# Kernel tuning notes

Measured on AMD Instinct MI355X. Metric: run time of the kernel, lower is better.

## Reference

```python
import jax, jax.numpy as jnp
import numpy as np

N_NODES = 100000
N_EDGES = 1600000
IN_DIM, HID, OUT_DIM = 128, 64, 1


def _sage_conv(x, src, dst, wl, wr, b, num_nodes):
    # PyG SAGEConv (aggr='mean', root_weight=True):
    #   out = lin_l(mean_{j in N(i)} x_j) + lin_r(x_i), bias lives in lin_l
    msgs = x[src]                                                  # [E, d] gather
    agg = jax.ops.segment_sum(msgs, dst, num_segments=num_nodes)  # [N, d]
    deg = jax.ops.segment_sum(jnp.ones((src.shape[0],), x.dtype), dst,
                              num_segments=num_nodes)              # [N]
    agg = agg / jnp.maximum(deg, 1.0)[:, None]                     # mean aggregation
    return agg @ wl + x @ wr + b


def setup_inputs() -> dict:
    key = jax.random.key(0)
    ks = jax.random.split(key, 12)
    x = jax.random.normal(ks[0], (N_NODES, IN_DIM), dtype=jnp.float32)
    edge_index = jax.random.randint(ks[1], (2, N_EDGES), 0, N_NODES, dtype=jnp.int64)

    def glorot(k, fan_in, fan_out):
        s = jnp.sqrt(2.0 / (fan_in + fan_out)).astype(jnp.float32)
        return jax.random.normal(k, (fan_in, fan_out), dtype=jnp.float32) * s

    return {
        "x": x,
        "edge_index": edge_index,
        "wl0": glorot(ks[2], IN_DIM, HID), "wr0": glorot(ks[3], IN_DIM, HID),
        "b0": jnp.zeros((HID,), jnp.float32),
        "wl1": glorot(ks[4], HID, HID), "wr1": glorot(ks[5], HID, HID),
        "b1": jnp.zeros((HID,), jnp.float32),
        "wl2": glorot(ks[6], HID, OUT_DIM), "wr2": glorot(ks[7], HID, OUT_DIM),
        "b2": jnp.zeros((OUT_DIM,), jnp.float32),
    }


def reference(x, edge_index, wl0, wr0, b0, wl1, wr1, b1, wl2, wr2, b2):
    src, dst = edge_index[0], edge_index[1]
    n = x.shape[0]
    # layer 0: conv -> relu (dropout is identity in eval mode)
    h = jax.nn.relu(_sage_conv(x, src, dst, wl0, wr0, b0, n))
    # layer 1
    h = jax.nn.relu(_sage_conv(h, src, dst, wl1, wr1, b1, n))
    # final layer + sigmoid
    h = _sage_conv(h, src, dst, wl2, wr2, b2, n)
    return jax.nn.sigmoid(h)
```

## Files before the change

### kernel.cpp

```cpp
#include <hip/hip_runtime.h>
#include <hip/hip_bf16.h>
#include <math.h>


#define SHIFT 7
#define BKT 128
#define CHUNK 4096
#define CAP 4096

typedef __bf16 bf16_t;
typedef bf16_t bf16x8 __attribute__((ext_vector_type(8)));
typedef float f32x4 __attribute__((ext_vector_type(4)));

#define B16LO(u) __uint_as_float((u) << 16)
#define B16HI(u) __uint_as_float((u) & 0xffff0000u)

__global__ __launch_bounds__(256) void scatter_prep(const int* __restrict__ srcv,
                                                    const int* __restrict__ dstv,
                                                    int* __restrict__ bcnt,
                                                    int* __restrict__ bucketed,
                                                    int E, int NB, int nbC,
                                                    const float* __restrict__ wl0,
                                                    const float* __restrict__ wr0,
                                                    const float* __restrict__ wl1,
                                                    const float* __restrict__ wr1,
                                                    bf16_t* __restrict__ w0t,
                                                    bf16_t* __restrict__ w1t) {
    if ((int)blockIdx.x >= nbC) {
        int idx = (blockIdx.x - nbC) * 256 + threadIdx.x;
        if (idx < 128 * 128) {
            int j = idx >> 7, k = idx & 127;
            float v = (j < 64) ? wl0[k * 64 + j] : wr0[k * 64 + (j - 64)];
            w0t[idx] = (bf16_t)v;
        } else if (idx < 128 * 128 + 128 * 64) {
            int i2 = idx - 128 * 128;
            int j = i2 >> 6, k = i2 & 63;
            float v = (j < 64) ? wl1[k * 64 + j] : wr1[k * 64 + (j - 64)];
            w1t[i2] = (bf16_t)v;
        }
        return;
    }
    __shared__ int hist[1024];
    __shared__ int offl[1024];
    __shared__ int basel[1024];
    __shared__ int partial[256];
    __shared__ int posA[CHUNK];
    __shared__ int valA[CHUNK];
    const int t = threadIdx.x;
    for (int i = t; i < NB; i += 256) hist[i] = 0;
    __syncthreads();

    const int cbase = blockIdx.x * CHUNK;
    int bk[CHUNK / 256], rk[CHUNK / 256], vv[CHUNK / 256];
#pragma unroll
    for (int k = 0; k < CHUNK / 256; ++k) {
        int e = cbase + t + k * 256;
        if (e < E) {
            int d = dstv[e];
            int s = srcv[e];
            int b = d >> SHIFT;
            bk[k] = b;
            rk[k] = atomicAdd(&hist[b], 1);
            vv[k] = (s << SHIFT) | (d & (BKT - 1));
        } else {
            bk[k] = -1;
        }
    }
    __syncthreads();

    for (int b = t; b < NB; b += 256) {
        int c = hist[b];
        basel[b] = c ? (b * CAP + atomicAdd(&bcnt[b], c)) : 0;
    }
    {
        int g = t * 4;
        int a0 = (g + 0 < NB) ? hist[g + 0] : 0;
        int a1 = (g + 1 < NB) ? hist[g + 1] : 0;
        int a2 = (g + 2 < NB) ? hist[g + 2] : 0;
        int a3 = (g + 3 < NB) ? hist[g + 3] : 0;
        int sum = a0 + a1 + a2 + a3;
        partial[t] = sum;
        __syncthreads();
        for (int d = 1; d < 256; d <<= 1) {
            int x = (t >= d) ? partial[t - d] : 0;
            __syncthreads();
            partial[t] += x;
            __syncthreads();
        }
        int ex = partial[t] - sum;
        if (g + 0 < NB) offl[g + 0] = ex;
        if (g + 1 < NB) offl[g + 1] = ex + a0;
        if (g + 2 < NB) offl[g + 2] = ex + a0 + a1;
        if (g + 3 < NB) offl[g + 3] = ex + a0 + a1 + a2;
    }
    __syncthreads();

    int nloc = E - cbase;
    if (nloc > CHUNK) nloc = CHUNK;
#pragma unroll
    for (int k = 0; k < CHUNK / 256; ++k) {
        if (bk[k] >= 0) {
            int slot = offl[bk[k]] + rk[k];
            posA[slot] = basel[bk[k]] + rk[k];
            valA[slot] = vv[k];
        }
    }
    __syncthreads();
    for (int j = t; j < nloc; j += 256) bucketed[posA[j]] = valA[j];
}

__global__ __launch_bounds__(256) void sort_gemm0(const int* __restrict__ bucketed,
                                                  const int* __restrict__ bcnt,
                                                  int2* __restrict__ od,
                                                  int* __restrict__ csr, int N, int NB,
                                                  const float* __restrict__ x,
                                                  const bf16_t* __restrict__ w0t,
                                                  bf16_t* __restrict__ y) {
    __shared__ int cnt[BKT];
    __shared__ int sc[BKT];
    __shared__ int cur[BKT];
    const int t = threadIdx.x;

    if ((int)blockIdx.x >= NB) {
        const int bid = blockIdx.x - NB;
        const int lane = t & 63;
        const int wv = t >> 6;
        const int r0 = bid * 64 + wv * 16;
        const int rr = lane & 15;
        const int quad = lane >> 4;
        const int row_store = r0 + rr;
        int row = (row_store < N) ? row_store : (N - 1);

        bf16x8 xf[4];
#pragma unroll
        for (int kk = 0; kk < 4; ++kk) {
            const float* ap = &x[(size_t)row * 128 + kk * 32 + quad * 8];
            float4 f0 = *(const float4*)ap;
            float4 f1 = *(const float4*)(ap + 4);
            union { bf16x8 v; bf16_t h[8]; } u;
            u.h[0] = (bf16_t)f0.x; u.h[1] = (bf16_t)f0.y;
            u.h[2] = (bf16_t)f0.z; u.h[3] = (bf16_t)f0.w;
            u.h[4] = (bf16_t)f1.x; u.h[5] = (bf16_t)f1.y;
            u.h[6] = (bf16_t)f1.z; u.h[7] = (bf16_t)f1.w;
            xf[kk] = u.v;
        }
#pragma unroll
        for (int c = 0; c < 8; ++c) {
            f32x4 acc = {0.f, 0.f, 0.f, 0.f};
#pragma unroll
            for (int kk = 0; kk < 4; ++kk) {
                bf16x8 wf = *(const bf16x8*)&w0t[(size_t)(c * 16 + rr) * 128 + kk * 32 + quad * 8];
                acc = __builtin_amdgcn_mfma_f32_16x16x32_bf16(wf, xf[kk], acc, 0, 0, 0);
            }
            if (row_store < N) {
                union { bf16_t h[4]; uint2 u; } p;
                p.h[0] = (bf16_t)acc[0]; p.h[1] = (bf16_t)acc[1];
                p.h[2] = (bf16_t)acc[2]; p.h[3] = (bf16_t)acc[3];
                *(uint2*)&y[(size_t)row_store * 128 + c * 16 + quad * 4] = p.u;
            }
        }
        return;
    }

    const int b = blockIdx.x;
    const int ebase = b * CAP;
    const int eend = ebase + bcnt[b];
    if (t < BKT) cnt[t] = 0;
    __syncthreads();
    int wreg[CAP / 256];
#pragma unroll
    for (int k = 0; k < CAP / 256; ++k) {
        int i = ebase + t + k * 256;
        if (i < eend) {
            wreg[k] = bucketed[i];
            atomicAdd(&cnt[wreg[k] & (BKT - 1)], 1);
        }
    }
    __syncthreads();
    int v = (t < BKT) ? cnt[t] : 0;
    if (t < BKT) sc[t] = v;
    __syncthreads();
    for (int d = 1; d < BKT; d <<= 1) {
        int xsc = (t < BKT && t >= d) ? sc[t - d] : 0;
        __syncthreads();
        if (t < BKT) sc[t] += xsc;
        __syncthreads();
    }
    if (t < BKT) {
        int ex = sc[t] - v;
        cur[t] = ex;
        int dst = (b << SHIFT) + t;
        if (dst < N) od[dst] = make_int2(ebase + ex, v);
    }
    __syncthreads();
#pragma unroll
    for (int k = 0; k < CAP / 256; ++k) {
        int i = ebase + t + k * 256;
        if (i < eend) {
            int w = wreg[k];
            int p = atomicAdd(&cur[w & (BKT - 1)], 1);
            csr[ebase + p] = w >> SHIFT;
        }
    }
}

__global__ __launch_bounds__(256) void gemm1(const bf16_t* __restrict__ A,
                                             const bf16_t* __restrict__ Wt,
                                             bf16_t* __restrict__ Y, int N) {
    const int lane = threadIdx.x & 63;
    const int wv = threadIdx.x >> 6;
    const int r0 = blockIdx.x * 64 + wv * 16;
    const int rr = lane & 15;
    const int quad = lane >> 4;
    const int row_store = r0 + rr;
    int row = (row_store < N) ? row_store : (N - 1);

    bf16x8 xf[2];
#pragma unroll
    for (int kk = 0; kk < 2; ++kk)
        xf[kk] = *(const bf16x8*)&A[(size_t)row * 64 + kk * 32 + quad * 8];

#pragma unroll
    for (int c = 0; c < 8; ++c) {
        f32x4 acc = {0.f, 0.f, 0.f, 0.f};
#pragma unroll
        for (int kk = 0; kk < 2; ++kk) {
            bf16x8 wf = *(const bf16x8*)&Wt[(size_t)(c * 16 + rr) * 64 + kk * 32 + quad * 8];
            acc = __builtin_amdgcn_mfma_f32_16x16x32_bf16(wf, xf[kk], acc, 0, 0, 0);
        }
        if (row_store < N) {
            union { bf16_t h[4]; uint2 u; } p;
            p.h[0] = (bf16_t)acc[0]; p.h[1] = (bf16_t)acc[1];
            p.h[2] = (bf16_t)acc[2]; p.h[3] = (bf16_t)acc[3];
            *(uint2*)&Y[(size_t)row_store * 128 + c * 16 + quad * 4] = p.u;
        }
    }
}

template <bool FUSED>
__global__ __launch_bounds__(256) void agg_relu(const bf16_t* __restrict__ y,
                                                const int* __restrict__ csr,
                                                const int2* __restrict__ od,
                                                const float* __restrict__ bias,
                                                bf16_t* __restrict__ h,
                                                const float* __restrict__ wl2,
                                                const float* __restrict__ wr2,
                                                float* __restrict__ sl,
                                                float* __restrict__ sr, int N) {
    const int lane = threadIdx.x & 63;
    const int oct = lane >> 3;
    const int ch = (lane & 7) * 8;
    const int nw = gridDim.x * 4;

    int i = blockIdx.x * 4 + (threadIdx.x >> 6);
    int2 odc = (i < N) ? od[i] : make_int2(0, 0);
    int sidx = 0;
    if (i < N) sidx = (lane < odc.y) ? csr[odc.x + lane] : 0;

    while (i < N) {
        const int inext = i + nw;
        int2 odn = (inext < N) ? od[inext] : make_int2(0, 0);

        const int base = odc.x;
        const int d = odc.y;
        float a0 = 0.f, a1 = 0.f, a2 = 0.f, a3 = 0.f;
        float a4 = 0.f, a5 = 0.f, a6 = 0.f, a7 = 0.f;
        const int nblk = d >> 3;
        const int pm = (nblk < 8) ? nblk : 8;
        int p = 0;
        for (; p + 2 <= pm; p += 2) {
            int s0 = __shfl(sidx, 8 * p + oct);
            int s1 = __shfl(sidx, 8 * p + 8 + oct);
            uint4 v0 = *(const uint4*)&y[(size_t)s0 * 128 + ch];
            uint4 v1 = *(const uint4*)&y[(size_t)s1 * 128 + ch];
            a0 += B16LO(v0.x) + B16LO(v1.x); a1 += B16HI(v0.x) + B16HI(v1.x);
            a2 += B16LO(v0.y) + B16LO(v1.y); a3 += B16HI(v0.y) + B16HI(v1.y);
            a4 += B16LO(v0.z) + B16LO(v1.z); a5 += B16HI(v0.z) + B16HI(v1.z);
            a6 += B16LO(v0.w) + B16LO(v1.w); a7 += B16HI(v0.w) + B16HI(v1.w);
        }
        for (; p < pm; ++p) {
            int s0 = __shfl(sidx, 8 * p + oct);
            uint4 v0 = *(const uint4*)&y[(size_t)s0 * 128 + ch];
            a0 += B16LO(v0.x); a1 += B16HI(v0.x);
            a2 += B16LO(v0.y); a3 += B16HI(v0.y);
            a4 += B16LO(v0.z); a5 += B16HI(v0.z);
            a6 += B16LO(v0.w); a7 += B16HI(v0.w);
        }
        for (; p < nblk; ++p) {
            int s0 = csr[base + 8 * p + oct];
            uint4 v0 = *(const uint4*)&y[(size_t)s0 * 128 + ch];
            a0 += B16LO(v0.x); a1 += B16HI(v0.x);
            a2 += B16LO(v0.y); a3 += B16HI(v0.y);
            a4 += B16LO(v0.z); a5 += B16HI(v0.z);
            a6 += B16LO(v0.w); a7 += B16HI(v0.w);
        }
        {
            int te = 8 * nblk + oct;
            int tec = (te < 64) ? te : 63;
            int s_t = __shfl(sidx, tec);
            if (te < d) {
                int s0 = (te < 64) ? s_t : csr[base + te];
                uint4 v0 = *(const uint4*)&y[(size_t)s0 * 128 + ch];
                a0 += B16LO(v0.x); a1 += B16HI(v0.x);
                a2 += B16LO(v0.y); a3 += B16HI(v0.y);
                a4 += B16LO(v0.z); a5 += B16HI(v0.z);
                a6 += B16LO(v0.w); a7 += B16HI(v0.w);
            }
        }

        int sidxn = 0;
        if (inext < N) sidxn = (lane < odn.y) ? csr[odn.x + lane] : 0;

        a0 += __shfl_xor(a0, 8);  a1 += __shfl_xor(a1, 8);
        a2 += __shfl_xor(a2, 8);  a3 += __shfl_xor(a3, 8);
        a4 += __shfl_xor(a4, 8);  a5 += __shfl_xor(a5, 8);
        a6 += __shfl_xor(a6, 8);  a7 += __shfl_xor(a7, 8);
        a0 += __shfl_xor(a0, 16); a1 += __shfl_xor(a1, 16);
        a2 += __shfl_xor(a2, 16); a3 += __shfl_xor(a3, 16);
        a4 += __shfl_xor(a4, 16); a5 += __shfl_xor(a5, 16);
        a6 += __shfl_xor(a6, 16); a7 += __shfl_xor(a7, 16);
        a0 += __shfl_xor(a0, 32); a1 += __shfl_xor(a1, 32);
        a2 += __shfl_xor(a2, 32); a3 += __shfl_xor(a3, 32);
        a4 += __shfl_xor(a4, 32); a5 += __shfl_xor(a5, 32);
        a6 += __shfl_xor(a6, 32); a7 += __shfl_xor(a7, 32);

        float inv = 1.f / ((d > 0) ? (float)d : 1.f);
        uint4 vs = *(const uint4*)&y[(size_t)i * 128 + 64 + ch];
        float4 bv0 = *(const float4*)&bias[ch];
        float4 bv1 = *(const float4*)&bias[ch + 4];
        float v0 = fmaxf(a0 * inv + B16LO(vs.x) + bv0.x, 0.f);
        float v1 = fmaxf(a1 * inv + B16HI(vs.x) + bv0.y, 0.f);
        float v2 = fmaxf(a2 * inv + B16LO(vs.y) + bv0.z, 0.f);
        float v3 = fmaxf(a3 * inv + B16HI(vs.y) + bv0.w, 0.f);
        float v4 = fmaxf(a4 * inv + B16LO(vs.z) + bv1.x, 0.f);
        float v5 = fmaxf(a5 * inv + B16HI(vs.z) + bv1.y, 0.f);
        float v6 = fmaxf(a6 * inv + B16LO(vs.w) + bv1.z, 0.f);
        float v7 = fmaxf(a7 * inv + B16HI(vs.w) + bv1.w, 0.f);

        if (!FUSED) {
            if (oct == 0) {
                union { bf16_t b[8]; uint4 u; } pk;
                pk.b[0] = (bf16_t)v0; pk.b[1] = (bf16_t)v1;
                pk.b[2] = (bf16_t)v2; pk.b[3] = (bf16_t)v3;
                pk.b[4] = (bf16_t)v4; pk.b[5] = (bf16_t)v5;
                pk.b[6] = (bf16_t)v6; pk.b[7] = (bf16_t)v7;
                *(uint4*)&h[(size_t)i * 64 + ch] = pk.u;
            }
        } else {
            float4 w0 = *(const float4*)&wl2[ch];
            float4 w1 = *(const float4*)&wl2[ch + 4];
            float4 u0 = *(const float4*)&wr2[ch];
            float4 u1 = *(const float4*)&wr2[ch + 4];
            float a = v0 * w0.x + v1 * w0.y + v2 * w0.z + v3 * w0.w +
                      v4 * w1.x + v5 * w1.y + v6 * w1.z + v7 * w1.w;
            float b = v0 * u0.x + v1 * u0.y + v2 * u0.z + v3 * u0.w +
                      v4 * u1.x + v5 * u1.y + v6 * u1.z + v7 * u1.w;
            a += __shfl_xor(a, 1); b += __shfl_xor(b, 1);
            a += __shfl_xor(a, 2); b += __shfl_xor(b, 2);
            a += __shfl_xor(a, 4); b += __shfl_xor(b, 4);
            if (lane == 0) { sl[i] = a; sr[i] = b; }
        }

        odc = odn;
        sidx = sidxn;
        i = inext;
    }
}

__global__ __launch_bounds__(256) void final_k(const float* __restrict__ sl,
                                               const float* __restrict__ sr,
                                               const int* __restrict__ csr,
                                               const int2* __restrict__ od,
                                               const float* __restrict__ b2,
                                               float* __restrict__ out, int N) {
    int wid = blockIdx.x * 4 + (threadIdx.x >> 6);
    if (wid >= N) return;
    const int lane = threadIdx.x & 63;
    const int2 odv = od[wid];
    const int base = odv.x;
    const int d = odv.y;
    float acc = 0.f;
    for (int e = lane; e < d; e += 64) acc += sl[csr[base + e]];
#pragma unroll
    for (int off = 32; off; off >>= 1) acc += __shfl_xor(acc, off);
    if (lane == 0) {
        float m = (d > 0) ? (float)d : 1.f;
        float v = acc / m + sr[wid] + b2[0];
        out[wid] = 1.f / (1.f + expf(-v));
    }
}

extern "C" void kernel_launch(void* const* d_in, const int* in_sizes, int n_in,
                              void* d_out, int out_size, void* d_ws, size_t ws_size,
                              hipStream_t stream) {
    const float* x  = (const float*)d_in[0];
    const int*  ei  = (const int*)d_in[1];
    const float* wl0 = (const float*)d_in[2];
    const float* wr0 = (const float*)d_in[3];
    const float* b0  = (const float*)d_in[4];
    const float* wl1 = (const float*)d_in[5];
    const float* wr1 = (const float*)d_in[6];
    const float* b1  = (const float*)d_in[7];
    const float* wl2 = (const float*)d_in[8];
    const float* wr2 = (const float*)d_in[9];
    const float* b2  = (const float*)d_in[10];
    float* out = (float*)d_out;

    const int E = in_sizes[1] / 2;
    const int N = out_size;
    const int* srcv = ei;
    const int* dstv = ei + E;
    const int NB = (N + BKT - 1) >> SHIFT;

    char* ws = (char*)d_ws;
    size_t o = 0;
    auto take = [&](size_t nbytes) -> void* {
        void* p = ws + o;
        o = (o + nbytes + 255) & ~(size_t)255;
        return p;
    };
    int2* od      = (int2*)take((size_t)N * 8);
    int* bcnt     = (int*)take((size_t)(NB + 2) * 4);
    int* bucketed = (int*)take((size_t)NB * CAP * 4);
    int* csr      = (int*)take((size_t)NB * CAP * 4);
    bf16_t* w0t   = (bf16_t*)take(128 * 128 * 2);
    bf16_t* w1t   = (bf16_t*)take(128 * 64 * 2);
    bf16_t* y     = (bf16_t*)take((size_t)N * 128 * 2);
    bf16_t* h     = (bf16_t*)take((size_t)N * 64 * 2);
    float* sl     = (float*)take((size_t)N * 4);
    float* sr     = (float*)take((size_t)N * 4);
    (void)ws_size;

    const int nbC = (E + CHUNK - 1) / CHUNK;
    const int nbP = (128 * 128 + 128 * 64 + 255) / 256;
    const int nbW = (N + 3) / 4;
    const int nbG = (N + 63) / 64;
    const int nbA = 2048;

    hipMemsetAsync(bcnt, 0, (size_t)NB * 4, stream);
    scatter_prep<<<nbC + nbP, 256, 0, stream>>>(srcv, dstv, bcnt, bucketed, E, NB, nbC,
                                                wl0, wr0, wl1, wr1, w0t, w1t);
    sort_gemm0<<<NB + nbG, 256, 0, stream>>>(bucketed, bcnt, od, csr, N, NB,
                                             x, w0t, y);

    agg_relu<false><<<nbA, 256, 0, stream>>>(y, csr, od, b0, h,
                                             nullptr, nullptr, nullptr, nullptr, N);
    gemm1<<<nbG, 256, 0, stream>>>(h, w1t, y, N);
    agg_relu<true><<<nbA, 256, 0, stream>>>(y, csr, od, b1, nullptr,
                                            wl2, wr2, sl, sr, N);
    final_k<<<nbW, 256, 0, stream>>>(sl, sr, csr, od, b2, out, N);
}
```

Measured before the change: 295.3 us.

## Fuse layer-0 aggregation with layer-1 GEMM through shared memory

Merges the layer-0 mean aggregation + ReLU kernel with the following layer-1 MFMA GEMM. Each block aggregates 64 nodes, staging the bf16 hidden rows in padded LDS, then multiplies them by the layer-1 weights and writes into a separate y2 buffer. This removes one kernel launch and the global write and read of the intermediate h, which also avoids the in-place hazard of reusing y. In exchange the aggregation now uses a fixed one-node-per-wave-iteration grid of N/64 blocks instead of the 2048-block grid-stride loop, which may change latency hiding.

```diff
diff --git a/kernel.cpp b/kernel.cpp
--- a/kernel.cpp
+++ b/kernel.cpp
@@ -7,6 +7,7 @@
 #define BKT 128
 #define CHUNK 4096
 #define CAP 4096
+#define HSTR 72
 
 typedef __bf16 bf16_t;
 typedef bf16_t bf16x8 __attribute__((ext_vector_type(8)));
@@ -204,28 +205,139 @@
     }
 }
 
-__global__ __launch_bounds__(256) void gemm1(const bf16_t* __restrict__ A,
-                                             const bf16_t* __restrict__ Wt,
-                                             bf16_t* __restrict__ Y, int N) {
-    const int lane = threadIdx.x & 63;
-    const int wv = threadIdx.x >> 6;
-    const int r0 = blockIdx.x * 64 + wv * 16;
+__global__ __launch_bounds__(256) void agg0_gemm1(const bf16_t* __restrict__ y,
+                                                  const int* __restrict__ csr,
+                                                  const int2* __restrict__ od,
+                                                  const float* __restrict__ bias,
+                                                  const bf16_t* __restrict__ w1t,
+                                                  bf16_t* __restrict__ Y, int N) {
+    __shared__ bf16_t hlds[64 * HSTR];
+    const int t = threadIdx.x;
+    const int lane = t & 63;
+    const int wv = t >> 6;
+    const int oct = lane >> 3;
+    const int ch = (lane & 7) * 8;
+    const int gbase = blockIdx.x * 64;
+    const int n0 = gbase + wv * 16;
+
+    const float4 bv0 = *(const float4*)&bias[ch];
+    const float4 bv1 = *(const float4*)&bias[ch + 4];
+
+    int i = n0;
+    int2 odc = (i < N) ? od[i] : make_int2(0, 0);
+    int sidx = 0;
+    if (i < N && lane < odc.y) sidx = csr[odc.x + lane];
+
+    for (int k = 0; k < 16; ++k) {
+        const int inext = n0 + k + 1;
+        const bool pf = (k < 15) && (inext < N);
+        int2 odn = pf ? od[inext] : make_int2(0, 0);
+
+        const int base = odc.x;
+        const int d = (i < N) ? odc.y : 0;
+        float a0 = 0.f, a1 = 0.f, a2 = 0.f, a3 = 0.f;
+        float a4 = 0.f, a5 = 0.f, a6 = 0.f, a7 = 0.f;
+        const int nblk = d >> 3;
+        const int pm = (nblk < 8) ? nblk : 8;
+        int p = 0;
+        for (; p + 2 <= pm; p += 2) {
+            int s0 = __shfl(sidx, 8 * p + oct);
+            int s1 = __shfl(sidx, 8 * p + 8 + oct);
+            uint4 v0 = *(const uint4*)&y[(size_t)s0 * 128 + ch];
+            uint4 v1 = *(const uint4*)&y[(size_t)s1 * 128 + ch];
+            a0 += B16LO(v0.x) + B16LO(v1.x); a1 += B16HI(v0.x) + B16HI(v1.x);
+            a2 += B16LO(v0.y) + B16LO(v1.y); a3 += B16HI(v0.y) + B16HI(v1.y);
+            a4 += B16LO(v0.z) + B16LO(v1.z); a5 += B16HI(v0.z) + B16HI(v1.z);
+            a6 += B16LO(v0.w) + B16LO(v1.w); a7 += B16HI(v0.w) + B16HI(v1.w);
+        }
+        for (; p < pm; ++p) {
+            int s0 = __shfl(sidx, 8 * p + oct);
+            uint4 v0 = *(const uint4*)&y[(size_t)s0 * 128 + ch];
+            a0 += B16LO(v0.x); a1 += B16HI(v0.x);
+            a2 += B16LO(v0.y); a3 += B16HI(v0.y);
+            a4 += B16LO(v0.z); a5 += B16HI(v0.z);
+            a6 += B16LO(v0.w); a7 += B16HI(v0.w);
+        }
+        for (; p < nblk; ++p) {
+            int s0 = csr[base + 8 * p + oct];
+            uint4 v0 = *(const uint4*)&y[(size_t)s0 * 128 + ch];
+            a0 += B16LO(v0.x); a1 += B16HI(v0.x);
+            a2 += B16LO(v0.y); a3 += B16HI(v0.y);
+            a4 += B16LO(v0.z); a5 += B16HI(v0.z);
+            a6 += B16LO(v0.w); a7 += B16HI(v0.w);
+        }
+        {
+            int te = 8 * nblk + oct;
+            int tec = (te < 64) ? te : 63;
+            int s_t = __shfl(sidx, tec);
+            if (te < d) {
+                int s0 = (te < 64) ? s_t : csr[base + te];
+                uint4 v0 = *(const uint4*)&y[(size_t)s0 * 128 + ch];
+                a0 += B16LO(v0.x); a1 += B16HI(v0.x);
+                a2 += B16LO(v0.y); a3 += B16HI(v0.y);
+                a4 += B16LO(v0.z); a5 += B16HI(v0.z);
+                a6 += B16LO(v0.w); a7 += B16HI(v0.w);
+            }
+        }
+
+        int sidxn = 0;
+        if (pf && lane < odn.y) sidxn = csr[odn.x + lane];
+
+        a0 += __shfl_xor(a0, 8);  a1 += __shfl_xor(a1, 8);
+        a2 += __shfl_xor(a2, 8);  a3 += __shfl_xor(a3, 8);
+        a4 += __shfl_xor(a4, 8);  a5 += __shfl_xor(a5, 8);
+        a6 += __shfl_xor(a6, 8);  a7 += __shfl_xor(a7, 8);
+        a0 += __shfl_xor(a0, 16); a1 += __shfl_xor(a1, 16);
+        a2 += __shfl_xor(a2, 16); a3 += __shfl_xor(a3, 16);
+        a4 += __shfl_xor(a4, 16); a5 += __shfl_xor(a5, 16);
+        a6 += __shfl_xor(a6, 16); a7 += __shfl_xor(a7, 16);
+        a0 += __shfl_xor(a0, 32); a1 += __shfl_xor(a1, 32);
+        a2 += __shfl_xor(a2, 32); a3 += __shfl_xor(a3, 32);
+        a4 += __shfl_xor(a4, 32); a5 += __shfl_xor(a5, 32);
+        a6 += __shfl_xor(a6, 32); a7 += __shfl_xor(a7, 32);
+
+        if (i < N) {
+            float inv = 1.f / ((d > 0) ? (float)d : 1.f);
+            uint4 vs = *(const uint4*)&y[(size_t)i * 128 + 64 + ch];
+            float v0 = fmaxf(a0 * inv + B16LO(vs.x) + bv0.x, 0.f);
+            float v1 = fmaxf(a1 * inv + B16HI(vs.x) + bv0.y, 0.f);
+            float v2 = fmaxf(a2 * inv + B16LO(vs.y) + bv0.z, 0.f);
+            float v3 = fmaxf(a3 * inv + B16HI(vs.y) + bv0.w, 0.f);
+            float v4 = fmaxf(a4 * inv + B16LO(vs.z) + bv1.x, 0.f);
+            float v5 = fmaxf(a5 * inv + B16HI(vs.z) + bv1.y, 0.f);
+            float v6 = fmaxf(a6 * inv + B16LO(vs.w) + bv1.z, 0.f);
+            float v7 = fmaxf(a7 * inv + B16HI(vs.w) + bv1.w, 0.f);
+            if (oct == 0) {
+                union { bf16_t b[8]; uint4 u; } pk;
+                pk.b[0] = (bf16_t)v0; pk.b[1] = (bf16_t)v1;
+                pk.b[2] = (bf16_t)v2; pk.b[3] = (bf16_t)v3;
+                pk.b[4] = (bf16_t)v4; pk.b[5] = (bf16_t)v5;
+                pk.b[6] = (bf16_t)v6; pk.b[7] = (bf16_t)v7;
+                *(uint4*)&hlds[(wv * 16 + k) * HSTR + ch] = pk.u;
+            }
+        }
+
+        odc = odn;
+        sidx = sidxn;
+        i = inext;
+    }
+    __syncthreads();
+
     const int rr = lane & 15;
     const int quad = lane >> 4;
-    const int row_store = r0 + rr;
-    int row = (row_store < N) ? row_store : (N - 1);
+    const int row_store = gbase + wv * 16 + rr;
 
     bf16x8 xf[2];
 #pragma unroll
     for (int kk = 0; kk < 2; ++kk)
-        xf[kk] = *(const bf16x8*)&A[(size_t)row * 64 + kk * 32 + quad * 8];
+        xf[kk] = *(const bf16x8*)&hlds[(wv * 16 + rr) * HSTR + kk * 32 + quad * 8];
 
 #pragma unroll
     for (int c = 0; c < 8; ++c) {
         f32x4 acc = {0.f, 0.f, 0.f, 0.f};
 #pragma unroll
         for (int kk = 0; kk < 2; ++kk) {
-            bf16x8 wf = *(const bf16x8*)&Wt[(size_t)(c * 16 + rr) * 64 + kk * 32 + quad * 8];
+            bf16x8 wf = *(const bf16x8*)&w1t[(size_t)(c * 16 + rr) * 64 + kk * 32 + quad * 8];
             acc = __builtin_amdgcn_mfma_f32_16x16x32_bf16(wf, xf[kk], acc, 0, 0, 0);
         }
         if (row_store < N) {
@@ -237,16 +349,14 @@
     }
 }
 
-template <bool FUSED>
-__global__ __launch_bounds__(256) void agg_relu(const bf16_t* __restrict__ y,
-                                                const int* __restrict__ csr,
-                                                const int2* __restrict__ od,
-                                                const float* __restrict__ bias,
-                                                bf16_t* __restrict__ h,
-                                                const float* __restrict__ wl2,
-                                                const float* __restrict__ wr2,
-                                                float* __restrict__ sl,
-                                                float* __restrict__ sr, int N) {
+__global__ __launch_bounds__(256) void agg1(const bf16_t* __restrict__ y,
+                                            const int* __restrict__ csr,
+                                            const int2* __restrict__ od,
+                                            const float* __restrict__ bias,
+                                            const float* __restrict__ wl2,
+                                            const float* __restrict__ wr2,
+                                            float* __restrict__ sl,
+                                            float* __restrict__ sr, int N) {
     const int lane = threadIdx.x & 63;
     const int oct = lane >> 3;
     const int ch = (lane & 7) * 8;
@@ -337,16 +447,7 @@
         float v6 = fmaxf(a6 * inv + B16LO(vs.w) + bv1.z, 0.f);
         float v7 = fmaxf(a7 * inv + B16HI(vs.w) + bv1.w, 0.f);
 
-        if (!FUSED) {
-            if (oct == 0) {
-                union { bf16_t b[8]; uint4 u; } pk;
-                pk.b[0] = (bf16_t)v0; pk.b[1] = (bf16_t)v1;
-                pk.b[2] = (bf16_t)v2; pk.b[3] = (bf16_t)v3;
-                pk.b[4] = (bf16_t)v4; pk.b[5] = (bf16_t)v5;
-                pk.b[6] = (bf16_t)v6; pk.b[7] = (bf16_t)v7;
-                *(uint4*)&h[(size_t)i * 64 + ch] = pk.u;
-            }
-        } else {
+        {
             float4 w0 = *(const float4*)&wl2[ch];
             float4 w1 = *(const float4*)&wl2[ch + 4];
             float4 u0 = *(const float4*)&wr2[ch];
@@ -426,7 +527,7 @@
     bf16_t* w0t   = (bf16_t*)take(128 * 128 * 2);
     bf16_t* w1t   = (bf16_t*)take(128 * 64 * 2);
     bf16_t* y     = (bf16_t*)take((size_t)N * 128 * 2);
-    bf16_t* h     = (bf16_t*)take((size_t)N * 64 * 2);
+    bf16_t* y2    = (bf16_t*)take((size_t)N * 128 * 2);
     float* sl     = (float*)take((size_t)N * 4);
     float* sr     = (float*)take((size_t)N * 4);
     (void)ws_size;
@@ -443,10 +544,7 @@
     sort_gemm0<<<NB + nbG, 256, 0, stream>>>(bucketed, bcnt, od, csr, N, NB,
                                              x, w0t, y);
 
-    agg_relu<false><<<nbA, 256, 0, stream>>>(y, csr, od, b0, h,
-                                             nullptr, nullptr, nullptr, nullptr, N);
-    gemm1<<<nbG, 256, 0, stream>>>(h, w1t, y, N);
-    agg_relu<true><<<nbA, 256, 0, stream>>>(y, csr, od, b1, nullptr,
-                                            wl2, wr2, sl, sr, N);
+    agg0_gemm1<<<nbG, 256, 0, stream>>>(y, csr, od, b0, w1t, y2, N);
+    agg1<<<nbA, 256, 0, stream>>>(y2, csr, od, b1, wl2, wr2, sl, sr, N);
     final_k<<<nbW, 256, 0, stream>>>(sl, sr, csr, od, b2, out, N);
 }
```

Result: no change. 290.2 us, median of 2 (-1.7%).
